# Optimization experiments

Measured on AMD Instinct MI355X. Metric: run time of the kernel, lower is better.

## Reference

```python
import jax, jax.numpy as jnp
import numpy as np

B, S, D = 2, 2048, 512
E, K = 8, 2
H = 4 * D  # expert_dim
EPS = 1e-10


def setup_inputs() -> dict:
    key = jax.random.key(0)
    ks = jax.random.split(key, 5)
    scale = 1.0 / np.sqrt(D)
    return {
        "x": jax.random.normal(ks[0], (B, S, D), dtype=jnp.float32),
        "w_router": jax.random.normal(ks[1], (D, E), dtype=jnp.float32) * scale,
        "w_gate": jax.random.normal(ks[2], (D, E * H), dtype=jnp.float32) * scale,
        "w_up": jax.random.normal(ks[3], (D, E * H), dtype=jnp.float32) * scale,
        "w_down": jax.random.normal(ks[4], (H, D), dtype=jnp.float32) * (1.0 / np.sqrt(H)),
    }


def reference(x, w_router, w_gate, w_up, w_down):
    b, s, d = x.shape
    n = b * s
    xf = x.reshape(n, d)

    # Router: softmax over experts, pick top-k, renormalize
    router_probs = jax.nn.softmax(xf @ w_router, axis=-1)          # [N, E]
    top_p, top_i = jax.lax.top_k(router_probs, K)                  # [N, K]
    top_p = top_p / (top_p.sum(axis=-1, keepdims=True) + EPS)

    # Dense all-expert gate/up projections (as in original module)
    gate = jax.nn.silu(xf @ w_gate).reshape(n, E, H)               # [N, E, H]
    up = (xf @ w_up).reshape(n, E, H)                              # [N, E, H]

    # Gather per-token top-k expert slices and combine
    sel_gate = jnp.take_along_axis(gate, top_i[:, :, None], axis=1)  # [N, K, H]
    sel_up = jnp.take_along_axis(up, top_i[:, :, None], axis=1)      # [N, K, H]
    combined = jnp.sum(top_p[:, :, None] * sel_gate * sel_up, axis=1)  # [N, H]

    out = (combined @ w_down).reshape(b, s, d)

    # Load-balancing aux loss
    expert_probs = router_probs.mean(axis=0)                       # [E]
    lb_loss = E * jnp.sum(expert_probs * jnp.log(expert_probs * E + EPS))
    return out, lb_loss
```

## Files before the change

kernel.cpp:

```cpp
#include <hip/hip_runtime.h>
#include <hip/hip_bf16.h>

#define N_TOK 4096
#define D_DIM 512
#define E_NUM 8
#define H_DIM 2048
#define RB_NUM 256
#define TP_NUM 8704

typedef __attribute__((ext_vector_type(8))) short short8;
typedef __attribute__((ext_vector_type(4))) float f32x4;

__device__ inline short f2bs(float f) {
  __hip_bfloat16 h = __float2bfloat16(f);
  return *reinterpret_cast<short*>(&h);
}

__device__ inline void llds16(const short* g, short* l) {
  __builtin_amdgcn_global_load_lds(
      (const __attribute__((address_space(1))) void*)g,
      (__attribute__((address_space(3))) void*)l, 16, 0, 0);
}

__global__ void __launch_bounds__(256) prep_router_kernel(
    const float* __restrict__ wg, const float* __restrict__ wu,
    const float* __restrict__ wd, const float* __restrict__ x,
    const float* __restrict__ wr, short* __restrict__ wgb,
    short* __restrict__ wub, short* __restrict__ wdb, short* __restrict__ xb,
    int* __restrict__ cnt_blk, int* __restrict__ tok_bkt,
    float* __restrict__ p_bkt, float* __restrict__ psum_blk) {
  int u = blockIdx.x;
  int tid = threadIdx.x;

  if (u >= RB_NUM) {
    __shared__ float tbuf[64][33];
    int v = u - RB_NUM;
    const float* in;
    short* op;
    int R, C, c0, r0;
    if (v < 8192) {
      in = (v < 4096) ? wg : wu;
      op = (v < 4096) ? wgb : wub;
      int w = v & 4095;
      R = D_DIM; C = E_NUM * H_DIM;
      c0 = (w & 511) * 32; r0 = (w >> 9) * 64;
    } else {
      in = wd; op = wdb;
      int w = v - 8192;
      R = H_DIM; C = D_DIM;
      c0 = (w & 15) * 32; r0 = (w >> 4) * 64;
    }
    int cx = tid & 7, ry = tid >> 3;
#pragma unroll
    for (int p = 0; p < 2; ++p) {
      int row = ry + 32 * p;
      float4 vv = *(const float4*)&in[(size_t)(r0 + row) * C + c0 + cx * 4];
      tbuf[row][cx * 4 + 0] = vv.x;
      tbuf[row][cx * 4 + 1] = vv.y;
      tbuf[row][cx * 4 + 2] = vv.z;
      tbuf[row][cx * 4 + 3] = vv.w;
    }
    __syncthreads();
    int tx = tid & 31, ty = tid >> 5;
#pragma unroll
    for (int i = 0; i < 4; ++i) {
      int cl = ty + 8 * i;
      unsigned lo = (unsigned short)f2bs(tbuf[2 * tx][cl]);
      unsigned hi = (unsigned short)f2bs(tbuf[2 * tx + 1][cl]);
      ((int*)op)[(((size_t)(c0 + cl) * R) + r0) / 2 + tx] = (int)(lo | (hi << 16));
    }
    return;
  }

  __shared__ float wr_t[E_NUM * D_DIM];
  __shared__ int h_cnt[E_NUM];
  __shared__ float psh[E_NUM];
  int rb = u;
  for (int i = tid; i < D_DIM * E_NUM; i += 256)
    wr_t[(i & 7) * D_DIM + (i >> 3)] = wr[i];
  if (tid < E_NUM) { h_cnt[tid] = 0; psh[tid] = 0.f; }
  __syncthreads();

  int r = tid >> 4, pp = tid & 15;
  int t = rb * 16 + r;
  const float* xr0 = x + (size_t)t * D_DIM;
  short* xw0 = xb + (size_t)t * D_DIM;
  float acc[8] = {0, 0, 0, 0, 0, 0, 0, 0};
#pragma unroll
  for (int j = 0; j < 8; ++j) {
    int d = j * 64 + pp * 4;
    float4 xv = *(const float4*)(xr0 + d);
    short4 o;
    o.x = f2bs(xv.x); o.y = f2bs(xv.y); o.z = f2bs(xv.z); o.w = f2bs(xv.w);
    *(short4*)(xw0 + d) = o;
#pragma unroll
    for (int e = 0; e < 8; ++e) {
      float4 w = *(const float4*)&wr_t[e * D_DIM + d];
      acc[e] += xv.x * w.x + xv.y * w.y + xv.z * w.z + xv.w * w.w;
    }
  }
#pragma unroll
  for (int e = 0; e < 8; ++e) {
    acc[e] += __shfl_xor(acc[e], 1);
    acc[e] += __shfl_xor(acc[e], 2);
    acc[e] += __shfl_xor(acc[e], 4);
    acc[e] += __shfl_xor(acc[e], 8);
  }

  if (pp == 0) {
    float m = acc[0];
#pragma unroll
    for (int e = 1; e < 8; ++e) m = fmaxf(m, acc[e]);
    float p[8], s = 0.f;
#pragma unroll
    for (int e = 0; e < 8; ++e) { p[e] = expf(acc[e] - m); s += p[e]; }
    float inv = 1.f / s;
#pragma unroll
    for (int e = 0; e < 8; ++e) {
      p[e] *= inv;
      atomicAdd(&psh[e], p[e]);
    }
    int i0 = 0;
#pragma unroll
    for (int e = 1; e < 8; ++e) if (p[e] > p[i0]) i0 = e;
    int i1 = (i0 == 0) ? 1 : 0;
#pragma unroll
    for (int e = 0; e < 8; ++e) if (e != i0 && p[e] > p[i1]) i1 = e;
    float ps = p[i0] + p[i1] + 1e-10f;
    float q0 = p[i0] / ps, q1 = p[i1] / ps;
    int l0 = atomicAdd(&h_cnt[i0], 1);
    int l1 = atomicAdd(&h_cnt[i1], 1);
    tok_bkt[i0 * (RB_NUM * 16) + rb * 16 + l0] = t * 2 + 0;
    p_bkt[i0 * (RB_NUM * 16) + rb * 16 + l0] = q0;
    tok_bkt[i1 * (RB_NUM * 16) + rb * 16 + l1] = t * 2 + 1;
    p_bkt[i1 * (RB_NUM * 16) + rb * 16 + l1] = q1;
  }
  __syncthreads();
  if (tid < E_NUM) {
    cnt_blk[rb * 8 + tid] = h_cnt[tid];
    psum_blk[rb * 8 + tid] = psh[tid];
  }
}

__global__ void __launch_bounds__(256) route_pack_kernel(
    const int* __restrict__ cnt_blk, const int* __restrict__ tok_bkt,
    const float* __restrict__ p_bkt, int* __restrict__ dense_tok,
    float* __restrict__ dense_p, int* __restrict__ n_tot) {
  int e = blockIdx.x >> 4;
  int chunk = blockIdx.x & 15;
  int tid = threadIdx.x, lane = tid & 63, wid = tid >> 6;
  __shared__ int wsum[4];
  __shared__ int s_excl[16];
  __shared__ int s_cnt[16];
  int c = cnt_blk[tid * 8 + e];
  int inc = c;
#pragma unroll
  for (int ofs = 1; ofs < 64; ofs <<= 1) {
    int v = __shfl_up(inc, ofs);
    if (lane >= ofs) inc += v;
  }
  if (lane == 63) wsum[wid] = inc;
  __syncthreads();
  int pre = 0;
#pragma unroll
  for (int w = 0; w < 4; ++w) pre += (w < wid) ? wsum[w] : 0;
  int excl = inc + pre - c;
  if ((tid >> 4) == chunk) {
    s_excl[tid & 15] = excl;
    s_cnt[tid & 15] = c;
  }
  if (chunk == 0 && tid == 255) n_tot[e] = inc + pre;
  __syncthreads();
  int rbl = tid >> 4, i = tid & 15;
  int rb = chunk * 16 + rbl;
  if (i < s_cnt[rbl]) {
    int src = e * (RB_NUM * 16) + rb * 16 + i;
    int dst = e * N_TOK + s_excl[rbl] + i;
    dense_tok[dst] = tok_bkt[src];
    dense_p[dst] = p_bkt[src];
  }
}

__global__ void __launch_bounds__(256, 2) moe_gateup_kernel(
    const short* __restrict__ xb, const short* __restrict__ wg,
    const short* __restrict__ wu, const int* __restrict__ dense_tok,
    const float* __restrict__ dense_p, const int* __restrict__ n_tot,
    const float* __restrict__ psum_blk, short* __restrict__ act,
    float* __restrict__ out_loss) {
  int e = blockIdx.z;
  int tid = threadIdx.x;

  if (e == 8) {
    if (blockIdx.x || blockIdx.y) return;
    __shared__ float sums[8];
    if (tid < 8) sums[tid] = 0.f;
    __syncthreads();
#pragma unroll
    for (int ee = 0; ee < 8; ++ee)
      atomicAdd(&sums[ee], psum_blk[tid * 8 + ee]);
    __syncthreads();
    if (tid == 0) {
      float lb = 0.f;
#pragma unroll
      for (int ee = 0; ee < 8; ++ee) {
        float pe = sums[ee] / (float)N_TOK;
        lb += pe * logf(pe * 8.f + 1e-10f);
      }
      out_loss[0] = 8.f * lb;
    }
    return;
  }

  int n_e = n_tot[e];
  int rt = blockIdx.y;
  if (rt * 256 >= n_e) return;
  int h0 = blockIdx.x * 64;

  __shared__ __align__(16) short As[256 * 64];
  __shared__ __align__(16) short Bgs[64 * 64];
  __shared__ __align__(16) short Bus[64 * 64];
  __shared__ int s_row[256];
  __shared__ float s_pr[256];

  int lane = tid & 63, wid = tid >> 6;

  {
    int r = rt * 256 + tid;
    int srow = -1;
    float spr = 0.f;
    if (r < n_e) {
      srow = dense_tok[e * N_TOK + r];
      spr = dense_p[e * N_TOK + r];
    }
    s_row[tid] = srow;
    s_pr[tid] = spr;
  }
  __syncthreads();

  int cg = (lane & 7) ^ (lane >> 3);
  const short* baseA[8];
  const short* baseB[4];
#pragma unroll
  for (int jj = 0; jj < 8; ++jj) {
    int r = wid * 64 + jj * 8 + (lane >> 3);
    int row = s_row[r];
    int t = (row < 0) ? 0 : (row >> 1);
    baseA[jj] = xb + (size_t)t * D_DIM + cg * 8;
  }
  short* ldsB;
  {
    const short* wB = ((wid & 2) ? wu : wg) + (size_t)e * H_DIM * D_DIM;
    int rb = (wid & 1) * 32;
    ldsB = ((wid & 2) ? Bus : Bgs) + rb * 64;
#pragma unroll
    for (int jj = 0; jj < 4; ++jj) {
      int h = h0 + rb + jj * 8 + (lane >> 3);
      baseB[jj] = wB + (size_t)h * D_DIM + cg * 8;
    }
  }

  int ml = lane & 15, quad = lane >> 4;
  int m0w = wid * 64;
  f32x4 accG[4][4], accU[4][4];
#pragma unroll
  for (int mf = 0; mf < 4; ++mf)
#pragma unroll
    for (int nf = 0; nf < 4; ++nf) {
      accG[mf][nf] = (f32x4){0, 0, 0, 0};
      accU[mf][nf] = (f32x4){0, 0, 0, 0};
    }

  for (int kt = 0; kt < D_DIM / 64; ++kt) {
    int kb = kt * 64;
#pragma unroll
    for (int jj = 0; jj < 8; ++jj)
      llds16(baseA[jj] + kb, As + wid * 4096 + jj * 512);
#pragma unroll
    for (int jj = 0; jj < 4; ++jj)
      llds16(baseB[jj] + kb, ldsB + jj * 512);
    __syncthreads();
#pragma unroll
    for (int ks = 0; ks < 2; ++ks) {
      int cs = ((quad + ks * 4) ^ (ml & 7)) * 8;
      short8 a[4], bg[4], bu[4];
#pragma unroll
      for (int mf = 0; mf < 4; ++mf)
        a[mf] = *(const short8*)&As[(m0w + mf * 16 + ml) * 64 + cs];
#pragma unroll
      for (int nf = 0; nf < 4; ++nf) {
        bg[nf] = *(const short8*)&Bgs[(nf * 16 + ml) * 64 + cs];
        bu[nf] = *(const short8*)&Bus[(nf * 16 + ml) * 64 + cs];
      }
#pragma unroll
      for (int mf = 0; mf < 4; ++mf)
#pragma unroll
        for (int nf = 0; nf < 4; ++nf) {
          accG[mf][nf] = __builtin_amdgcn_mfma_f32_16x16x32_bf16(a[mf], bg[nf], accG[mf][nf], 0, 0, 0);
          accU[mf][nf] = __builtin_amdgcn_mfma_f32_16x16x32_bf16(a[mf], bu[nf], accU[mf][nf], 0, 0, 0);
        }
    }
    __syncthreads();
  }

#pragma unroll
  for (int mf = 0; mf < 4; ++mf)
#pragma unroll
    for (int r = 0; r < 4; ++r) {
      int rl = m0w + mf * 16 + quad * 4 + r;
      int arow = s_row[rl];
      if (arow >= 0) {
        float pr = s_pr[rl];
#pragma unroll
        for (int nf = 0; nf < 4; ++nf) {
          float g = accG[mf][nf][r], u = accU[mf][nf][r];
          float val = pr * (g / (1.f + __expf(-g))) * u;
          act[(size_t)arow * H_DIM + h0 + nf * 16 + ml] = f2bs(val);
        }
      }
    }
}

__global__ void __launch_bounds__(256, 3) down_kernel(
    const short* __restrict__ act, const short* __restrict__ wd,
    float* __restrict__ partial) {
  __shared__ __align__(16) short As0[64 * 64];
  __shared__ __align__(16) short As1[64 * 64];
  __shared__ __align__(16) short Bs[256 * 64];
  int d0 = blockIdx.x * 256;
  int t0 = blockIdx.y * 64;
  int ksb = blockIdx.z;
  int tid = threadIdx.x, lane = tid & 63, wid = tid >> 6;
  int cg = (lane & 7) ^ (lane >> 3);

  const short* baseA[4];
  const short* baseB[8];
  int slot = wid >> 1;
  int arow0 = (wid & 1) * 32;
#pragma unroll
  for (int jj = 0; jj < 4; ++jj) {
    int r = arow0 + jj * 8 + (lane >> 3);
    baseA[jj] = act + (size_t)(2 * (t0 + r) + slot) * H_DIM + cg * 8;
  }
#pragma unroll
  for (int jj = 0; jj < 8; ++jj) {
    int d = d0 + wid * 64 + jj * 8 + (lane >> 3);
    baseB[jj] = wd + (size_t)d * H_DIM + cg * 8;
  }
  short* ldsA = (slot ? As1 : As0) + arow0 * 64;

  int ml = lane & 15, quad = lane >> 4;
  int n0w = wid * 64;
  f32x4 acc[4][4];
#pragma unroll
  for (int mf = 0; mf < 4; ++mf)
#pragma unroll
    for (int nf = 0; nf < 4; ++nf) acc[mf][nf] = (f32x4){0, 0, 0, 0};

  for (int j = 0; j < 8; ++j) {
    int hb = (ksb * 8 + j) * 64;
#pragma unroll
    for (int jj = 0; jj < 4; ++jj)
      llds16(baseA[jj] + hb, ldsA + jj * 512);
#pragma unroll
    for (int jj = 0; jj < 8; ++jj)
      llds16(baseB[jj] + hb, Bs + wid * 4096 + jj * 512);
    __syncthreads();
#pragma unroll
    for (int ks = 0; ks < 2; ++ks) {
      int cs = ((quad + ks * 4) ^ (ml & 7)) * 8;
      short8 a0[4], a1[4], b[4];
#pragma unroll
      for (int mf = 0; mf < 4; ++mf) {
        a0[mf] = *(const short8*)&As0[(mf * 16 + ml) * 64 + cs];
        a1[mf] = *(const short8*)&As1[(mf * 16 + ml) * 64 + cs];
      }
#pragma unroll
      for (int nf = 0; nf < 4; ++nf)
        b[nf] = *(const short8*)&Bs[(n0w + nf * 16 + ml) * 64 + cs];
#pragma unroll
      for (int mf = 0; mf < 4; ++mf)
#pragma unroll
        for (int nf = 0; nf < 4; ++nf) {
          acc[mf][nf] = __builtin_amdgcn_mfma_f32_16x16x32_bf16(a0[mf], b[nf], acc[mf][nf], 0, 0, 0);
          acc[mf][nf] = __builtin_amdgcn_mfma_f32_16x16x32_bf16(a1[mf], b[nf], acc[mf][nf], 0, 0, 0);
        }
    }
    __syncthreads();
  }

  float* pout = partial + (size_t)ksb * N_TOK * D_DIM;
#pragma unroll
  for (int mf = 0; mf < 4; ++mf)
#pragma unroll
    for (int r = 0; r < 4; ++r) {
      int t = t0 + mf * 16 + quad * 4 + r;
#pragma unroll
      for (int nf = 0; nf < 4; ++nf)
        pout[(size_t)t * D_DIM + d0 + n0w + nf * 16 + ml] = acc[mf][nf][r];
    }
}

__global__ void __launch_bounds__(256) reduce_kernel(
    const float* __restrict__ partial, float* __restrict__ out) {
  int i = blockIdx.x * 256 + threadIdx.x;
  const int Q = N_TOK * D_DIM / 4;
  const float4* p = (const float4*)partial;
  float4 a = p[i], b = p[i + Q], c = p[i + 2 * Q], d = p[i + 3 * Q];
  float4 r = {a.x + b.x + c.x + d.x, a.y + b.y + c.y + d.y,
              a.z + b.z + c.z + d.z, a.w + b.w + c.w + d.w};
  ((float4*)out)[i] = r;
}

extern "C" void kernel_launch(void* const* d_in, const int* in_sizes, int n_in,
                              void* d_out, int out_size, void* d_ws, size_t ws_size,
                              hipStream_t stream) {
  const float* x = (const float*)d_in[0];
  const float* wr = (const float*)d_in[1];
  const float* wg = (const float*)d_in[2];
  const float* wu = (const float*)d_in[3];
  const float* wd = (const float*)d_in[4];
  float* out = (float*)d_out;

  char* ws = (char*)d_ws;
  size_t off = 0;
  auto alloc = [&](size_t bytes) {
    char* p = ws + off;
    off += (bytes + 255) & ~(size_t)255;
    return p;
  };
  short* xb = (short*)alloc((size_t)N_TOK * D_DIM * 2);
  short* wgb = (short*)alloc((size_t)E_NUM * H_DIM * D_DIM * 2);
  short* wub = (short*)alloc((size_t)E_NUM * H_DIM * D_DIM * 2);
  short* wdb = (short*)alloc((size_t)D_DIM * H_DIM * 2);
  short* act = (short*)alloc((size_t)N_TOK * 2 * H_DIM * 2);
  float* partial = (float*)alloc((size_t)4 * N_TOK * D_DIM * 4);
  int* cnt_blk = (int*)alloc((size_t)RB_NUM * E_NUM * 4);
  int* tok_bkt = (int*)alloc((size_t)E_NUM * RB_NUM * 16 * 4);
  float* p_bkt = (float*)alloc((size_t)E_NUM * RB_NUM * 16 * 4);
  float* psum_blk = (float*)alloc((size_t)RB_NUM * E_NUM * 4);
  int* dense_tok = (int*)alloc((size_t)E_NUM * N_TOK * 4);
  float* dense_p = (float*)alloc((size_t)E_NUM * N_TOK * 4);
  int* n_tot = (int*)alloc((size_t)E_NUM * 4);

  prep_router_kernel<<<RB_NUM + TP_NUM, 256, 0, stream>>>(
      wg, wu, wd, x, wr, wgb, wub, wdb, xb, cnt_blk, tok_bkt, p_bkt, psum_blk);
  route_pack_kernel<<<E_NUM * 16, 256, 0, stream>>>(
      cnt_blk, tok_bkt, p_bkt, dense_tok, dense_p, n_tot);
  moe_gateup_kernel<<<dim3(H_DIM / 64, N_TOK / 256, E_NUM + 1), 256, 0, stream>>>(
      xb, wgb, wub, dense_tok, dense_p, n_tot, psum_blk, act,
      out + (size_t)N_TOK * D_DIM);
  down_kernel<<<dim3(D_DIM / 256, N_TOK / 64, 4), 256, 0, stream>>>(
      act, wdb, partial);
  reduce_kernel<<<N_TOK * D_DIM / 4 / 256, 256, 0, stream>>>(partial, out);
}
```

Measured before the change: 202.0 us.

## Store down-projection split-K partials as bf16 and remap block order

The down kernel now writes its split-K partial sums as bf16 instead of fp32, and the reduce kernel reads bf16 partials with 8-wide vector loads and widens them back to float. This halves the partial buffer traffic on both the write and the read side. The 3D grid is also replaced by a 1D grid with a grouped block-index remap, so blocks that share the same act rows run close together. Rounding the partials to bf16 before summation adds precision loss to the output.

```diff
diff --git a/kernel.cpp b/kernel.cpp
--- a/kernel.cpp
+++ b/kernel.cpp
@@ -322,13 +322,18 @@
 
 __global__ void __launch_bounds__(256, 3) down_kernel(
     const short* __restrict__ act, const short* __restrict__ wd,
-    float* __restrict__ partial) {
+    short* __restrict__ partial) {
+  int bid = blockIdx.x;
+  int g = bid >> 4, rr = bid & 15;
+  int m = rr >> 3;
+  int p = g * 8 + (rr & 7);
+  int d0 = m * 256;
+  int t0 = (p & 63) * 64;
+  int ksb = p >> 6;
+
   __shared__ __align__(16) short As0[64 * 64];
   __shared__ __align__(16) short As1[64 * 64];
   __shared__ __align__(16) short Bs[256 * 64];
-  int d0 = blockIdx.x * 256;
-  int t0 = blockIdx.y * 64;
-  int ksb = blockIdx.z;
   int tid = threadIdx.x, lane = tid & 63, wid = tid >> 6;
   int cg = (lane & 7) ^ (lane >> 3);
 
@@ -388,7 +393,7 @@
     __syncthreads();
   }
 
-  float* pout = partial + (size_t)ksb * N_TOK * D_DIM;
+  short* pout = partial + (size_t)ksb * N_TOK * D_DIM;
 #pragma unroll
   for (int mf = 0; mf < 4; ++mf)
 #pragma unroll
@@ -396,19 +401,30 @@
       int t = t0 + mf * 16 + quad * 4 + r;
 #pragma unroll
       for (int nf = 0; nf < 4; ++nf)
-        pout[(size_t)t * D_DIM + d0 + n0w + nf * 16 + ml] = acc[mf][nf][r];
+        pout[(size_t)t * D_DIM + d0 + n0w + nf * 16 + ml] = f2bs(acc[mf][nf][r]);
     }
 }
 
 __global__ void __launch_bounds__(256) reduce_kernel(
-    const float* __restrict__ partial, float* __restrict__ out) {
+    const short* __restrict__ partial, float* __restrict__ out) {
   int i = blockIdx.x * 256 + threadIdx.x;
-  const int Q = N_TOK * D_DIM / 4;
-  const float4* p = (const float4*)partial;
-  float4 a = p[i], b = p[i + Q], c = p[i + 2 * Q], d = p[i + 3 * Q];
-  float4 r = {a.x + b.x + c.x + d.x, a.y + b.y + c.y + d.y,
-              a.z + b.z + c.z + d.z, a.w + b.w + c.w + d.w};
-  ((float4*)out)[i] = r;
+  const int Q = N_TOK * D_DIM / 8;
+  float s[8];
+#pragma unroll
+  for (int j = 0; j < 8; ++j) s[j] = 0.f;
+#pragma unroll
+  for (int k = 0; k < 4; ++k) {
+    short8 v = ((const short8*)partial)[i + k * Q];
+#pragma unroll
+    for (int j = 0; j < 8; ++j) {
+      unsigned u = (unsigned)(unsigned short)v[j] << 16;
+      s[j] += *reinterpret_cast<float*>(&u);
+    }
+  }
+  float4 lo = {s[0], s[1], s[2], s[3]};
+  float4 hi = {s[4], s[5], s[6], s[7]};
+  ((float4*)out)[i * 2] = lo;
+  ((float4*)out)[i * 2 + 1] = hi;
 }
 
 extern "C" void kernel_launch(void* const* d_in, const int* in_sizes, int n_in,
@@ -433,7 +449,7 @@
   short* wub = (short*)alloc((size_t)E_NUM * H_DIM * D_DIM * 2);
   short* wdb = (short*)alloc((size_t)D_DIM * H_DIM * 2);
   short* act = (short*)alloc((size_t)N_TOK * 2 * H_DIM * 2);
-  float* partial = (float*)alloc((size_t)4 * N_TOK * D_DIM * 4);
+  short* partial = (short*)alloc((size_t)4 * N_TOK * D_DIM * 2);
   int* cnt_blk = (int*)alloc((size_t)RB_NUM * E_NUM * 4);
   int* tok_bkt = (int*)alloc((size_t)E_NUM * RB_NUM * 16 * 4);
   float* p_bkt = (float*)alloc((size_t)E_NUM * RB_NUM * 16 * 4);
@@ -449,7 +465,6 @@
   moe_gateup_kernel<<<dim3(H_DIM / 64, N_TOK / 256, E_NUM + 1), 256, 0, stream>>>(
       xb, wgb, wub, dense_tok, dense_p, n_tot, psum_blk, act,
       out + (size_t)N_TOK * D_DIM);
-  down_kernel<<<dim3(D_DIM / 256, N_TOK / 64, 4), 256, 0, stream>>>(
-      act, wdb, partial);
-  reduce_kernel<<<N_TOK * D_DIM / 4 / 256, 256, 0, stream>>>(partial, out);
-}
+  down_kernel<<<512, 256, 0, stream>>>(act, wdb, partial);
+  reduce_kernel<<<N_TOK * D_DIM / 8 / 256, 256, 0, stream>>>(partial, out);
+}
```

Result: no change. 200.8 us (-0.6%).
